# Kernel tuning notes

Hardware: AMD Instinct MI355X
Metric: run time of the kernel (lower is better)

Reference implementation:

```python
import jax, jax.numpy as jnp
from jax import lax
import numpy as np

H = 16   # num_heads
K = 31   # kernel_size
P = 15   # padding_l (left padding for 'same')


def setup_inputs() -> dict:
    key = jax.random.key(0)
    k1, k2, k3 = jax.random.split(key, 3)
    T, B, C = 2048, 32, 512
    x = jax.random.normal(k1, (T, B, C), dtype=jnp.float32)
    # xavier-uniform-ish init for (H, 1, K)
    limit = float(np.sqrt(6.0 / (1 + K)))
    weight = jax.random.uniform(k2, (H, 1, K), dtype=jnp.float32, minval=-limit, maxval=limit)
    bias = jnp.zeros((C,), dtype=jnp.float32)
    return {"x": x, "weight": weight, "bias": bias}


def reference(x, weight, bias):
    # x: (T, B, C); weight: (H, 1, K); bias: (C,)
    T, B, C = x.shape
    R = C // H  # channels per head
    w = weight.reshape(H, K)
    # weight_softmax=True: softmax over kernel dim in fp32, cast back
    w = jax.nn.softmax(w.astype(jnp.float32), axis=1).astype(weight.dtype)
    # expand per-head weights to per-channel depthwise kernel (C, 1, K)
    wc = jnp.repeat(w, R, axis=0)[:, None, :]
    x_bct = jnp.transpose(x, (1, 2, 0))  # (B, C, T)
    # out[b,c,t] = sum_k wc[c,0,k] * x[b,c,t - P + k], zero-padded
    out = lax.conv_general_dilated(
        x_bct, wc,
        window_strides=(1,),
        padding=[(P, K - 1 - P)],
        feature_group_count=C,
        dimension_numbers=("NCH", "OIH", "NCH"),
    )  # (B, C, T)
    out = jnp.transpose(out, (2, 0, 1))  # (T, B, C)
    return out + bias[None, None, :]
```

## Files before the change

kernel.cpp:

```cpp
#include <hip/hip_runtime.h>

#define T_DIM 2048
#define B_DIM 32
#define C_DIM 512
#define H_DIM 16
#define K_DIM 31
#define P_PAD 15
#define SEG 32
#define SEGLEN (T_DIM / SEG)
#define TT 8
#define WIN (TT + K_DIM - 1)
#define STRIDE (B_DIM * C_DIM)

__global__ __launch_bounds__(256, 8)
void lwconv_kernel(const float* __restrict__ x, const float* __restrict__ weight,
                   const float* __restrict__ bias, float* __restrict__ out)
{
    const int wid  = __builtin_amdgcn_readfirstlane((int)(threadIdx.x >> 6));
    const int lane = threadIdx.x & 63;
    const int g    = blockIdx.x * 4 + wid;
    const int h    = g & (H_DIM - 1);
    const int bp   = (g >> 4) & 15;
    const int seg  = g >> 8;
    const int c    = (h << 5) | (lane & 31);
    const int b    = (bp << 1) | (lane >> 5);

    float w[K_DIM];
    float m = -3.4e38f;
    #pragma unroll
    for (int k = 0; k < K_DIM; ++k) { w[k] = weight[h * K_DIM + k]; m = fmaxf(m, w[k]); }
    float s = 0.f;
    #pragma unroll
    for (int k = 0; k < K_DIM; ++k) { w[k] = __expf(w[k] - m); s += w[k]; }
    const float inv = 1.f / s;
    unsigned int ws[K_DIM];
    #pragma unroll
    for (int k = 0; k < K_DIM; ++k)
        ws[k] = __builtin_amdgcn_readfirstlane(__float_as_uint(w[k] * inv));

    const float bv = bias[c];
    const float* xp = x + (size_t)b * C_DIM + c;
    float*       op = out + (size_t)b * C_DIM + c;
    const int t0 = seg * SEGLEN;

    float xw[WIN];
    #pragma unroll
    for (int i = 0; i < K_DIM - 1; ++i) {
        int t = t0 - P_PAD + i;
        xw[i] = (t >= 0) ? xp[(size_t)t * STRIDE] : 0.f;
    }

    #pragma unroll 1
    for (int chunk = 0; chunk < SEGLEN / TT; ++chunk) {
        const int tb = t0 + chunk * TT;
        #pragma unroll
        for (int i = 0; i < TT; ++i) {
            int t = tb + P_PAD + i;
            xw[K_DIM - 1 + i] = (t < T_DIM) ? xp[(size_t)t * STRIDE] : 0.f;
        }
        #pragma unroll
        for (int i = 0; i < TT; ++i) {
            float acc = bv;
            #pragma unroll
            for (int k = 0; k < K_DIM; ++k)
                acc = fmaf(__uint_as_float(ws[k]), xw[i + k], acc);
            op[(size_t)(tb + i) * STRIDE] = acc;
        }
        #pragma unroll
        for (int i = 0; i < WIN - TT; ++i) xw[i] = xw[i + TT];
    }
}

extern "C" void kernel_launch(void* const* d_in, const int* in_sizes, int n_in,
                              void* d_out, int out_size, void* d_ws, size_t ws_size,
                              hipStream_t stream) {
    const float* x      = (const float*)d_in[0];
    const float* weight = (const float*)d_in[1];
    const float* bias   = (const float*)d_in[2];
    float* out = (float*)d_out;
    dim3 grid(H_DIM * 16 * SEG / 4);
    dim3 block(256);
    lwconv_kernel<<<grid, block, 0, stream>>>(x, weight, bias, out);
}
```

Baseline: 61.28 us.

## Replace sliding-window loop with scatter-accumulate over 32-step time tiles

Each wave now handles one 32-step time tile instead of a 64-step segment processed in chunks of 8. Each loaded input row is scattered into up to 32 register accumulators, and the tile is fully unrolled with no window shifting. The grid grows to 64 tiles along time, which raises parallelism. The cost is more halo reloads: 62 loads per 32 outputs instead of 94 per 64. It also keeps 32 accumulators live, which raises register pressure under the 8-waves launch bound.

```diff
diff --git a/kernel.cpp b/kernel.cpp
--- a/kernel.cpp
+++ b/kernel.cpp
@@ -6,11 +6,9 @@
 #define H_DIM 16
 #define K_DIM 31
 #define P_PAD 15
-#define SEG 32
-#define SEGLEN (T_DIM / SEG)
-#define TT 8
-#define WIN (TT + K_DIM - 1)
-#define STRIDE (B_DIM * C_DIM)
+#define TT 32
+#define JN (TT + K_DIM - 1)
+#define NCOL (B_DIM * C_DIM)
 
 __global__ __launch_bounds__(256, 8)
 void lwconv_kernel(const float* __restrict__ x, const float* __restrict__ weight,
@@ -18,12 +16,13 @@
 {
     const int wid  = __builtin_amdgcn_readfirstlane((int)(threadIdx.x >> 6));
     const int lane = threadIdx.x & 63;
-    const int g    = blockIdx.x * 4 + wid;
-    const int h    = g & (H_DIM - 1);
-    const int bp   = (g >> 4) & 15;
-    const int seg  = g >> 8;
+    const int gw   = blockIdx.x * 4 + wid;
+    const int h    = gw & (H_DIM - 1);
+    const int bp   = (gw >> 4) & 15;
+    const int tblk = gw >> 8;
     const int c    = (h << 5) | (lane & 31);
     const int b    = (bp << 1) | (lane >> 5);
+    const int col  = b * C_DIM + c;
 
     float w[K_DIM];
     float m = -3.4e38f;
@@ -39,36 +38,30 @@
         ws[k] = __builtin_amdgcn_readfirstlane(__float_as_uint(w[k] * inv));
 
     const float bv = bias[c];
-    const float* xp = x + (size_t)b * C_DIM + c;
-    float*       op = out + (size_t)b * C_DIM + c;
-    const int t0 = seg * SEGLEN;
+    const int tb = tblk * TT;
+    const float* xp = x + col;
+    float*       op = out + col;
 
-    float xw[WIN];
+    float acc[TT];
     #pragma unroll
-    for (int i = 0; i < K_DIM - 1; ++i) {
-        int t = t0 - P_PAD + i;
-        xw[i] = (t >= 0) ? xp[(size_t)t * STRIDE] : 0.f;
+    for (int i = 0; i < TT; ++i) acc[i] = bv;
+
+    #pragma unroll
+    for (int j = 0; j < JN; ++j) {
+        const int t  = tb - P_PAD + j;
+        int tc = t < 0 ? 0 : (t >= T_DIM ? T_DIM - 1 : t);
+        float v = xp[(size_t)tc * NCOL];
+        if (t < 0 || t >= T_DIM) v = 0.f;
+        const int ilo = (j - (K_DIM - 1)) > 0 ? (j - (K_DIM - 1)) : 0;
+        const int ihi = j < (TT - 1) ? j : (TT - 1);
+        #pragma unroll
+        for (int i = ilo; i <= ihi; ++i)
+            acc[i] = fmaf(__uint_as_float(ws[j - i]), v, acc[i]);
     }
 
-    #pragma unroll 1
-    for (int chunk = 0; chunk < SEGLEN / TT; ++chunk) {
-        const int tb = t0 + chunk * TT;
-        #pragma unroll
-        for (int i = 0; i < TT; ++i) {
-            int t = tb + P_PAD + i;
-            xw[K_DIM - 1 + i] = (t < T_DIM) ? xp[(size_t)t * STRIDE] : 0.f;
-        }
-        #pragma unroll
-        for (int i = 0; i < TT; ++i) {
-            float acc = bv;
-            #pragma unroll
-            for (int k = 0; k < K_DIM; ++k)
-                acc = fmaf(__uint_as_float(ws[k]), xw[i + k], acc);
-            op[(size_t)(tb + i) * STRIDE] = acc;
-        }
-        #pragma unroll
-        for (int i = 0; i < WIN - TT; ++i) xw[i] = xw[i + TT];
-    }
+    #pragma unroll
+    for (int i = 0; i < TT; ++i)
+        op[(size_t)(tb + i) * NCOL] = acc[i];
 }
 
 extern "C" void kernel_launch(void* const* d_in, const int* in_sizes, int n_in,
@@ -78,7 +71,7 @@
     const float* weight = (const float*)d_in[1];
     const float* bias   = (const float*)d_in[2];
     float* out = (float*)d_out;
-    dim3 grid(H_DIM * 16 * SEG / 4);
+    dim3 grid(H_DIM * 16 * (T_DIM / TT) / 4);
     dim3 block(256);
     lwconv_kernel<<<grid, block, 0, stream>>>(x, weight, bias, out);
 }
```

Result: slower. 94.17 us (+53.7%).
